# Kernel tuning notes

Measured on AMD Instinct MI355X. Metric: run time of the kernel, lower is better.

The kernel has to match this reference:

```python
import jax, jax.numpy as jnp
import numpy as np

B, C, H, W = 8, 128, 256, 256
KERNELS = [1, 3, 5]


def _dwconv(x, w, k):
    # depthwise conv, groups == channels, padding k//2 (SAME for odd k)
    return jax.lax.conv_general_dilated(
        x, w, window_strides=(1, 1),
        padding=[(k // 2, k // 2), (k // 2, k // 2)],
        dimension_numbers=("NCHW", "OIHW", "NCHW"),
        feature_group_count=x.shape[1])


def setup_inputs() -> dict:
    key = jax.random.key(0)
    ks = jax.random.split(key, 5)
    x = jax.random.normal(ks[0], (B, C, H, W), jnp.float32)
    # depthwise weights: torch layout [out_ch, in_ch/groups, k, k] = [4C, 1, k, k]
    w1 = jax.random.normal(ks[1], (4 * C, 1, 1, 1), jnp.float32) * 0.2
    w3 = jax.random.normal(ks[2], (4 * C, 1, 3, 3), jnp.float32) * 0.1
    w5 = jax.random.normal(ks[3], (4 * C, 1, 5, 5), jnp.float32) * 0.05
    # proj 1x1 conv: [4C, 12C, 1, 1]
    w_proj = jax.random.normal(ks[4], (4 * C, 12 * C, 1, 1), jnp.float32) * 0.02
    return {"x": x, "w1": w1, "w3": w3, "w5": w5, "w_proj": w_proj}


def reference(x, w1, w3, w5, w_proj):
    # DWT: strided split -> channel concat  [B,C,H,W] -> [B,4C,H/2,W/2]
    xd = jnp.concatenate([
        x[:, :, 0::2, 0::2], x[:, :, 0::2, 1::2],
        x[:, :, 1::2, 0::2], x[:, :, 1::2, 1::2]], axis=1)
    # multi-kernel depthwise convs, concat -> [B,12C,H/2,W/2]
    feats = jnp.concatenate([
        _dwconv(xd, w1, 1), _dwconv(xd, w3, 3), _dwconv(xd, w5, 5)], axis=1)
    # 1x1 projection: [B,12C,h,w] -> [B,4C,h,w]
    y = jnp.einsum("bchw,oc->bohw", feats, w_proj[:, :, 0, 0])
    # IDWT: strided zero-scatter back to [B,C,H,W]
    c = y.shape[1] // 4
    ll, lh, hl, hh = jnp.split(y, 4, axis=1)
    out = jnp.zeros((y.shape[0], c, y.shape[2] * 2, y.shape[3] * 2), y.dtype)
    out = (out.at[:, :, 0::2, 0::2].set(ll)
              .at[:, :, 0::2, 1::2].set(lh)
              .at[:, :, 1::2, 0::2].set(hl)
              .at[:, :, 1::2, 1::2].set(hh))
    return out
```

## Files before the change

kernel.cpp:

```cpp
#include <hip/hip_runtime.h>
#include <hip/hip_bf16.h>
#include <stdint.h>

typedef __bf16 bf16_t;
typedef __bf16 bf16x8 __attribute__((ext_vector_type(8)));
typedef float f32x4 __attribute__((ext_vector_type(4)));

constexpr int CC = 128, HH = 256, WW = 256;
constexpr int C4 = 512, K12 = 1536;
constexpr int AWP_ELEMS = 786432;
constexpr int LW2_ELEMS = 512 * 40;

__global__ __launch_bounds__(256)
void prep(const float* __restrict__ wp, const float* __restrict__ w1,
          const float* __restrict__ w3, const float* __restrict__ w5,
          bf16_t* __restrict__ awp, float* __restrict__ lw2g)
{
    int t = blockIdx.x * 256 + threadIdx.x;
    if (t < AWP_ELEMS) {
        int kk = t & 31, o = (t >> 5) & 511, t2 = t >> 14;
        int g = t2 >> 4, cb = t2 & 15;
        awp[t] = (bf16_t)wp[o * K12 + g * C4 + cb * 32 + kk];
        return;
    }
    int u = t - AWP_ELEMS;
    if (u < LW2_ELEMS) {
        int c4 = u / 40, j = u - c4 * 40;
        int r = j >> 3, v = j & 7;
        float val = 0.f;
        if (v < 5)                 val = w5[c4 * 25 + r * 5 + v];
        else if (r >= 1 && r <= 3) val = w3[c4 * 9 + (r - 1) * 3 + (v - 5)];
        else if (r == 0 && v == 5) val = w1[c4];
        lw2g[u] = val;
    }
}

__device__ __forceinline__ void gload4(const float* g, float* l) {
    __builtin_amdgcn_global_load_lds(
        (const __attribute__((address_space(1))) uint32_t*)g,
        (__attribute__((address_space(3))) uint32_t*)l, 4, 0, 0);
}
__device__ __forceinline__ uint16_t b16bits(float v) {
    return __builtin_bit_cast(uint16_t, (bf16_t)v);
}

__device__ __forceinline__ int bt_off(int row, int colbyte) {
    int f = ((row >> 1) ^ (row >> 2)) & 7;
    return row * 256 + (colbyte ^ (f << 4));
}

__global__ __launch_bounds__(1024, 4)
void wtconv_mfma(const float* __restrict__ x,
                 const bf16_t* __restrict__ awp,
                 const float* __restrict__ lw2g,
                 float* __restrict__ out)
{
    __shared__ __align__(16) float lx[32][5][136];
    __shared__ __align__(16) char  BtB[2][128 * 256];
    __shared__ __align__(16) float lw2s[32][40];

    const int tid = threadIdx.x;
    const int lane = tid & 63;
    const int wid = __builtin_amdgcn_readfirstlane(tid >> 6);
    const int nb = blockIdx.x;
    const int m = (nb & 7) * 128 + (nb >> 3);
    const int b = m >> 7, i = m & 127;
    const int wm = wid & 7, wn = wid >> 3;
    const int lrow = lane & 15, lkh = lane >> 4;
    const float* xb = x + (size_t)b * CC * HH * WW;

    for (int e = tid; e < 32 * 5 * 136 / 4; e += 1024)
        ((f32x4*)lx)[e] = (f32x4){0.f, 0.f, 0.f, 0.f};
    __syncthreads();

    f32x4 acc[4][4];
#pragma unroll
    for (int a = 0; a < 4; ++a)
#pragma unroll
        for (int c = 0; c < 4; ++c) acc[a][c] = (f32x4){0.f, 0.f, 0.f, 0.f};

    auto issue_own = [&](int kk) {
        const int q4 = kk >> 2, qy = q4 >> 1, qx = q4 & 1;
        const int bcb = (kk & 3) * 32;
#pragma unroll
        for (int cl = 0; cl < 2; ++cl) {
            const int chan = wid * 2 + cl;
#pragma unroll
            for (int r = 0; r < 5; ++r) {
                const int ri = i + r - 2;
                if ((unsigned)ri < 128u) {
                    const float* s = xb + (((size_t)(bcb + chan)) << 16)
                                   + (2 * ri + qy) * WW + qx;
                    gload4(s + 2 * lane,       &lx[chan][r][2]);
                    gload4(s + 128 + 2 * lane, &lx[chan][r][66]);
                }
            }
        }
        const float* wsrc = lw2g + kk * 1280 + wid * 80;
        float* wdst = &lw2s[wid * 2][0];
        gload4(wsrc + lane, wdst);
        if (lane < 16) gload4(wsrc + 64 + lane, wdst + 64);
    };

    issue_own(0);

    const int chan = tid >> 5;
    const int pxq = tid & 31;
    const int px0 = pxq * 4;

#pragma unroll 1
    for (int k = 0; k <= 16; ++k) {
        __syncthreads();

        if (k < 16) {
            const float* wr = &lw2s[chan][0];
            float f5[4] = {0.f,0.f,0.f,0.f}, f3[4] = {0.f,0.f,0.f,0.f}, f1[4];
            float w1v = 0.f;
#pragma unroll
            for (int r = 0; r < 5; ++r) {
                f32x4 wA = *(const f32x4*)(wr + r * 8);
                f32x4 wB = *(const f32x4*)(wr + r * 8 + 4);
                f32x4 a  = *(const f32x4*)&lx[chan][r][px0];
                f32x4 bv = *(const f32x4*)&lx[chan][r][px0 + 4];
                float c[8] = {a[0],a[1],a[2],a[3],bv[0],bv[1],bv[2],bv[3]};
                if (r == 0) w1v = wB[1];
#pragma unroll
                for (int d = 0; d < 4; ++d)
                    f5[d] += wA[0]*c[d] + wA[1]*c[d+1] + wA[2]*c[d+2]
                           + wA[3]*c[d+3] + wB[0]*c[d+4];
                if (r >= 1 && r <= 3) {
#pragma unroll
                    for (int d = 0; d < 4; ++d)
                        f3[d] += wB[1]*c[d+1] + wB[2]*c[d+2] + wB[3]*c[d+3];
                }
                if (r == 2) {
#pragma unroll
                    for (int d = 0; d < 4; ++d) f1[d] = w1v * c[d + 2];
                }
            }
            char* btb = BtB[k & 1];
            const int cby = chan * 2;
#pragma unroll
            for (int d = 0; d < 4; ++d) {
                const int row = px0 + d;
                const int sw = (((row >> 1) ^ (row >> 2)) & 7) << 4;
                char* base = btb + row * 256;
                *(uint16_t*)(base + ((cby) ^ sw))        = b16bits(f1[d]);
                *(uint16_t*)(base + ((64 + cby) ^ sw))   = b16bits(f3[d]);
                *(uint16_t*)(base + ((128 + cby) ^ sw))  = b16bits(f5[d]);
            }
            if (k < 15) issue_own(k + 1);
        }

        if (k > 0) {
            const int prev = k - 1;
            const char* btb = BtB[prev & 1];
#pragma unroll
            for (int s = 0; s < 3; ++s) {
                bf16x8 bfrag[4];
#pragma unroll
                for (int nf = 0; nf < 4; ++nf) {
                    const int row = wn * 64 + nf * 16 + lrow;
                    const int sw = (((row >> 1) ^ (row >> 2)) & 7) << 4;
                    bfrag[nf] = *(const bf16x8*)(btb + row * 256
                                                 + ((s * 64 + lkh * 16) ^ sw));
                }
                const bf16_t* abase = awp + (size_t)(s * 16 + prev) * (512 * 32);
#pragma unroll
                for (int mf = 0; mf < 4; ++mf) {
                    const int o = wm * 64 + mf * 16 + lrow;
                    bf16x8 af = *(const bf16x8*)(abase + o * 32 + lkh * 8);
#pragma unroll
                    for (int nf = 0; nf < 4; ++nf)
                        acc[mf][nf] = __builtin_amdgcn_mfma_f32_16x16x32_bf16(
                            af, bfrag[nf], acc[mf][nf], 0, 0, 0);
                }
            }
        }
    }

    const int oy = 2 * i + (wm >> 2);
    const int ox = (wm >> 1) & 1;
#pragma unroll
    for (int mf = 0; mf < 4; ++mf)
#pragma unroll
        for (int nf = 0; nf < 4; ++nf)
#pragma unroll
            for (int r = 0; r < 4; ++r) {
                const int bco = (wm & 1) * 64 + mf * 16 + lkh * 4 + r;
                const int px  = wn * 64 + nf * 16 + lrow;
                out[((size_t)(b * CC + bco) * HH + oy) * WW + 2 * px + ox]
                    = acc[mf][nf][r];
            }
}

extern "C" void kernel_launch(void* const* d_in, const int* in_sizes, int n_in,
                              void* d_out, int out_size, void* d_ws, size_t ws_size,
                              hipStream_t stream) {
    const float* x  = (const float*)d_in[0];
    const float* w1 = (const float*)d_in[1];
    const float* w3 = (const float*)d_in[2];
    const float* w5 = (const float*)d_in[3];
    const float* wp = (const float*)d_in[4];
    float* out = (float*)d_out;
    bf16_t* awp = (bf16_t*)d_ws;
    float* lw2g = (float*)((char*)d_ws + (size_t)AWP_ELEMS * 2);

    int prep_total = AWP_ELEMS + LW2_ELEMS;
    hipLaunchKernelGGL(prep, dim3((prep_total + 255) / 256), dim3(256), 0, stream,
                       wp, w1, w3, w5, awp, lw2g);
    hipLaunchKernelGGL(wtconv_mfma, dim3(1024), dim3(1024), 0, stream,
                       x, awp, lw2g, out);
}
```

Before: 514.8 us.

## Warp-specialize block: producer waves do dwconv plus partial MFMA, others MFMA only

Splits the 16 waves into two roles. Waves 0-7 load x tiles, compute the depthwise convolutions into the bf16 B tile, and handle 48 pixel columns of the projection GEMM. Waves 8-15 do only MFMA work on the remaining 80 columns, balancing the producers' extra load. It also changes the LDS swizzle pattern and raises wave priority around the MFMA sections with s_setprio. The aim is to overlap VALU conv work with matrix-core work, at the cost of uneven per-wave register use and a wider per-thread conv footprint.

Result: slower. 580.9 us (+12.9%).

```diff
diff --git a/kernel.cpp b/kernel.cpp
--- a/kernel.cpp
+++ b/kernel.cpp
@@ -43,10 +43,8 @@
 __device__ __forceinline__ uint16_t b16bits(float v) {
     return __builtin_bit_cast(uint16_t, (bf16_t)v);
 }
-
-__device__ __forceinline__ int bt_off(int row, int colbyte) {
-    int f = ((row >> 1) ^ (row >> 2)) & 7;
-    return row * 256 + (colbyte ^ (f << 4));
+__device__ __forceinline__ int btsw(int row) {
+    return (((row >> 1) ^ (row >> 3)) & 7) << 4;
 }
 
 __global__ __launch_bounds__(1024, 4)
@@ -65,7 +63,6 @@
     const int nb = blockIdx.x;
     const int m = (nb & 7) * 128 + (nb >> 3);
     const int b = m >> 7, i = m & 127;
-    const int wm = wid & 7, wn = wid >> 3;
     const int lrow = lane & 15, lkh = lane >> 4;
     const float* xb = x + (size_t)b * CC * HH * WW;
 
@@ -73,125 +70,180 @@
         ((f32x4*)lx)[e] = (f32x4){0.f, 0.f, 0.f, 0.f};
     __syncthreads();
 
-    f32x4 acc[4][4];
-#pragma unroll
-    for (int a = 0; a < 4; ++a)
-#pragma unroll
-        for (int c = 0; c < 4; ++c) acc[a][c] = (f32x4){0.f, 0.f, 0.f, 0.f};
-
-    auto issue_own = [&](int kk) {
-        const int q4 = kk >> 2, qy = q4 >> 1, qx = q4 & 1;
-        const int bcb = (kk & 3) * 32;
-#pragma unroll
-        for (int cl = 0; cl < 2; ++cl) {
-            const int chan = wid * 2 + cl;
-#pragma unroll
-            for (int r = 0; r < 5; ++r) {
-                const int ri = i + r - 2;
-                if ((unsigned)ri < 128u) {
-                    const float* s = xb + (((size_t)(bcb + chan)) << 16)
-                                   + (2 * ri + qy) * WW + qx;
-                    gload4(s + 2 * lane,       &lx[chan][r][2]);
-                    gload4(s + 128 + 2 * lane, &lx[chan][r][66]);
+    if (wid < 8) {
+        f32x4 acc[4][3];
+#pragma unroll
+        for (int a = 0; a < 4; ++a)
+#pragma unroll
+            for (int c = 0; c < 3; ++c) acc[a][c] = (f32x4){0.f, 0.f, 0.f, 0.f};
+
+        auto issue_own = [&](int kk) {
+            const int q4 = kk >> 2, qy = q4 >> 1, qx = q4 & 1;
+            const int bcb = (kk & 3) * 32;
+#pragma unroll
+            for (int cl = 0; cl < 4; ++cl) {
+                const int ch = wid * 4 + cl;
+#pragma unroll
+                for (int r = 0; r < 5; ++r) {
+                    const int ri = i + r - 2;
+                    if ((unsigned)ri < 128u) {
+                        const float* s = xb + (((size_t)(bcb + ch)) << 16)
+                                       + (2 * ri + qy) * WW + qx;
+                        gload4(s + 2 * lane,       &lx[ch][r][2]);
+                        gload4(s + 128 + 2 * lane, &lx[ch][r][66]);
+                    }
+                }
+            }
+            const float* wsrc = lw2g + kk * 1280 + wid * 160;
+            float* wdst = &lw2s[wid * 4][0];
+            gload4(wsrc + lane, wdst);
+            gload4(wsrc + 64 + lane, wdst + 64);
+            if (lane < 32) gload4(wsrc + 128 + lane, wdst + 128);
+        };
+        issue_own(0);
+
+        const int chan = wid * 4 + (lane >> 4);
+        const int oct = lane & 15;
+        const int px0 = oct * 8;
+
+#pragma unroll 1
+        for (int k = 0; k <= 16; ++k) {
+            __syncthreads();
+
+            if (k < 16) {
+                const float* wrow = &lw2s[chan][0];
+                float f5[8] = {0,0,0,0,0,0,0,0}, f3[8] = {0,0,0,0,0,0,0,0}, f1[8];
+                float w1v = 0.f;
+#pragma unroll
+                for (int r = 0; r < 5; ++r) {
+                    f32x4 wA = *(const f32x4*)(wrow + r * 8);
+                    f32x4 wB = *(const f32x4*)(wrow + r * 8 + 4);
+                    f32x4 v0 = *(const f32x4*)&lx[chan][r][px0];
+                    f32x4 v1 = *(const f32x4*)&lx[chan][r][px0 + 4];
+                    f32x4 v2 = *(const f32x4*)&lx[chan][r][px0 + 8];
+                    float cc[12] = {v0[0],v0[1],v0[2],v0[3], v1[0],v1[1],v1[2],v1[3],
+                                    v2[0],v2[1],v2[2],v2[3]};
+                    if (r == 0) w1v = wB[1];
+#pragma unroll
+                    for (int d = 0; d < 8; ++d)
+                        f5[d] += wA[0]*cc[d] + wA[1]*cc[d+1] + wA[2]*cc[d+2]
+                               + wA[3]*cc[d+3] + wB[0]*cc[d+4];
+                    if (r >= 1 && r <= 3) {
+#pragma unroll
+                        for (int d = 0; d < 8; ++d)
+                            f3[d] += wB[1]*cc[d+1] + wB[2]*cc[d+2] + wB[3]*cc[d+3];
+                    }
+                    if (r == 2) {
+#pragma unroll
+                        for (int d = 0; d < 8; ++d) f1[d] = w1v * cc[d + 2];
+                    }
+                }
+                char* btb = BtB[k & 1];
+                const int cby = chan * 2;
+#pragma unroll
+                for (int d = 0; d < 8; ++d) {
+                    const int row = px0 + d;
+                    char* base = btb + row * 256;
+                    const int sw = btsw(row);
+                    *(uint16_t*)(base + ((cby) ^ sw))       = b16bits(f1[d]);
+                    *(uint16_t*)(base + ((64 + cby) ^ sw))  = b16bits(f3[d]);
+                    *(uint16_t*)(base + ((128 + cby) ^ sw)) = b16bits(f5[d]);
+                }
+                if (k < 15) issue_own(k + 1);
+            }
+
+            if (k > 0) {
+                const int prev = k - 1;
+                const char* btb = BtB[prev & 1];
+#pragma unroll
+                for (int s = 0; s < 3; ++s) {
+                    bf16x8 bfrag[3];
+#pragma unroll
+                    for (int nf = 0; nf < 3; ++nf) {
+                        const int row = nf * 16 + lrow;
+                        bfrag[nf] = *(const bf16x8*)(btb + row * 256
+                                       + ((s * 64 + lkh * 16) ^ btsw(row)));
+                    }
+                    const bf16_t* abase = awp + (size_t)(s * 16 + prev) * (512 * 32);
+                    __builtin_amdgcn_s_setprio(1);
+#pragma unroll
+                    for (int mf = 0; mf < 4; ++mf) {
+                        const int o = wid * 64 + mf * 16 + lrow;
+                        bf16x8 af = *(const bf16x8*)(abase + o * 32 + lkh * 8);
+#pragma unroll
+                        for (int nf = 0; nf < 3; ++nf)
+                            acc[mf][nf] = __builtin_amdgcn_mfma_f32_16x16x32_bf16(
+                                af, bfrag[nf], acc[mf][nf], 0, 0, 0);
+                    }
+                    __builtin_amdgcn_s_setprio(0);
                 }
             }
         }
-        const float* wsrc = lw2g + kk * 1280 + wid * 80;
-        float* wdst = &lw2s[wid * 2][0];
-        gload4(wsrc + lane, wdst);
-        if (lane < 16) gload4(wsrc + 64 + lane, wdst + 64);
-    };
-
-    issue_own(0);
-
-    const int chan = tid >> 5;
-    const int pxq = tid & 31;
-    const int px0 = pxq * 4;
+        const int q = wid >> 1;
+        const int oy = 2 * i + (q >> 1), ox = q & 1;
+#pragma unroll
+        for (int mf = 0; mf < 4; ++mf)
+#pragma unroll
+            for (int nf = 0; nf < 3; ++nf)
+#pragma unroll
+                for (int r = 0; r < 4; ++r) {
+                    const int bco = (wid & 1) * 64 + mf * 16 + lkh * 4 + r;
+                    const int px  = nf * 16 + lrow;
+                    out[((size_t)(b * CC + bco) * HH + oy) * WW + 2 * px + ox]
+                        = acc[mf][nf][r];
+                }
+    } else {
+        f32x4 acc[4][5];
+#pragma unroll
+        for (int a = 0; a < 4; ++a)
+#pragma unroll
+            for (int c = 0; c < 5; ++c) acc[a][c] = (f32x4){0.f, 0.f, 0.f, 0.f};
+        const int wmB = wid - 8;
 
 #pragma unroll 1
-    for (int k = 0; k <= 16; ++k) {
-        __syncthreads();
-
-        if (k < 16) {
-            const float* wr = &lw2s[chan][0];
-            float f5[4] = {0.f,0.f,0.f,0.f}, f3[4] = {0.f,0.f,0.f,0.f}, f1[4];
-            float w1v = 0.f;
-#pragma unroll
-            for (int r = 0; r < 5; ++r) {
-                f32x4 wA = *(const f32x4*)(wr + r * 8);
-                f32x4 wB = *(const f32x4*)(wr + r * 8 + 4);
-                f32x4 a  = *(const f32x4*)&lx[chan][r][px0];
-                f32x4 bv = *(const f32x4*)&lx[chan][r][px0 + 4];
-                float c[8] = {a[0],a[1],a[2],a[3],bv[0],bv[1],bv[2],bv[3]};
-                if (r == 0) w1v = wB[1];
-#pragma unroll
-                for (int d = 0; d < 4; ++d)
-                    f5[d] += wA[0]*c[d] + wA[1]*c[d+1] + wA[2]*c[d+2]
-                           + wA[3]*c[d+3] + wB[0]*c[d+4];
-                if (r >= 1 && r <= 3) {
-#pragma unroll
-                    for (int d = 0; d < 4; ++d)
-                        f3[d] += wB[1]*c[d+1] + wB[2]*c[d+2] + wB[3]*c[d+3];
-                }
-                if (r == 2) {
-#pragma unroll
-                    for (int d = 0; d < 4; ++d) f1[d] = w1v * c[d + 2];
-                }
-            }
-            char* btb = BtB[k & 1];
-            const int cby = chan * 2;
-#pragma unroll
-            for (int d = 0; d < 4; ++d) {
-                const int row = px0 + d;
-                const int sw = (((row >> 1) ^ (row >> 2)) & 7) << 4;
-                char* base = btb + row * 256;
-                *(uint16_t*)(base + ((cby) ^ sw))        = b16bits(f1[d]);
-                *(uint16_t*)(base + ((64 + cby) ^ sw))   = b16bits(f3[d]);
-                *(uint16_t*)(base + ((128 + cby) ^ sw))  = b16bits(f5[d]);
-            }
-            if (k < 15) issue_own(k + 1);
+        for (int k = 0; k <= 16; ++k) {
+            __syncthreads();
+            if (k > 0) {
+                const int prev = k - 1;
+                const char* btb = BtB[prev & 1];
+#pragma unroll
+                for (int s = 0; s < 3; ++s) {
+                    bf16x8 bfrag[5];
+#pragma unroll
+                    for (int nf = 0; nf < 5; ++nf) {
+                        const int row = 48 + nf * 16 + lrow;
+                        bfrag[nf] = *(const bf16x8*)(btb + row * 256
+                                       + ((s * 64 + lkh * 16) ^ btsw(row)));
+                    }
+                    const bf16_t* abase = awp + (size_t)(s * 16 + prev) * (512 * 32);
+                    __builtin_amdgcn_s_setprio(1);
+#pragma unroll
+                    for (int mf = 0; mf < 4; ++mf) {
+                        const int o = wmB * 64 + mf * 16 + lrow;
+                        bf16x8 af = *(const bf16x8*)(abase + o * 32 + lkh * 8);
+#pragma unroll
+                        for (int nf = 0; nf < 5; ++nf)
+                            acc[mf][nf] = __builtin_amdgcn_mfma_f32_16x16x32_bf16(
+                                af, bfrag[nf], acc[mf][nf], 0, 0, 0);
+                    }
+                    __builtin_amdgcn_s_setprio(0);
+                }
+            }
         }
-
-        if (k > 0) {
-            const int prev = k - 1;
-            const char* btb = BtB[prev & 1];
-#pragma unroll
-            for (int s = 0; s < 3; ++s) {
-                bf16x8 bfrag[4];
-#pragma unroll
-                for (int nf = 0; nf < 4; ++nf) {
-                    const int row = wn * 64 + nf * 16 + lrow;
-                    const int sw = (((row >> 1) ^ (row >> 2)) & 7) << 4;
-                    bfrag[nf] = *(const bf16x8*)(btb + row * 256
-                                                 + ((s * 64 + lkh * 16) ^ sw));
-                }
-                const bf16_t* abase = awp + (size_t)(s * 16 + prev) * (512 * 32);
-#pragma unroll
-                for (int mf = 0; mf < 4; ++mf) {
-                    const int o = wm * 64 + mf * 16 + lrow;
-                    bf16x8 af = *(const bf16x8*)(abase + o * 32 + lkh * 8);
-#pragma unroll
-                    for (int nf = 0; nf < 4; ++nf)
-                        acc[mf][nf] = __builtin_amdgcn_mfma_f32_16x16x32_bf16(
-                            af, bfrag[nf], acc[mf][nf], 0, 0, 0);
-                }
-            }
-        }
+        const int q = wmB >> 1;
+        const int oy = 2 * i + (q >> 1), ox = q & 1;
+#pragma unroll
+        for (int mf = 0; mf < 4; ++mf)
+#pragma unroll
+            for (int nf = 0; nf < 5; ++nf)
+#pragma unroll
+                for (int r = 0; r < 4; ++r) {
+                    const int bco = (wmB & 1) * 64 + mf * 16 + lkh * 4 + r;
+                    const int px  = 48 + nf * 16 + lrow;
+                    out[((size_t)(b * CC + bco) * HH + oy) * WW + 2 * px + ox]
+                        = acc[mf][nf][r];
+                }
     }
-
-    const int oy = 2 * i + (wm >> 2);
-    const int ox = (wm >> 1) & 1;
-#pragma unroll
-    for (int mf = 0; mf < 4; ++mf)
-#pragma unroll
-        for (int nf = 0; nf < 4; ++nf)
-#pragma unroll
-            for (int r = 0; r < 4; ++r) {
-                const int bco = (wm & 1) * 64 + mf * 16 + lkh * 4 + r;
-                const int px  = wn * 64 + nf * 16 + lrow;
-                out[((size_t)(b * CC + bco) * HH + oy) * WW + 2 * px + ox]
-                    = acc[mf][nf][r];
-            }
 }
 
 extern "C" void kernel_launch(void* const* d_in, const int* in_sizes, int n_in,
```

## Specialize half the waves for depthwise conv and raise MFMA issue priority

Applied to the files above, without the earlier changes.

The depthwise-conv producer stage moves from all 16 waves to only the first 8. Each of those waves now loads 4 channels and computes 8 pixels per thread, while the other 8 waves only run MFMAs. The LDS swizzle for the B tile changes to match the new write pattern, and s_setprio brackets the MFMA section so matrix ops get issue priority. The aim is to reuse each loaded input window across more outputs and to overlap conv with MFMA. The risks are more register pressure, idle waves during the conv stage, and an imbalance between the two groups.

New measurement: 821.1 us. 1.6x slower.

```diff
diff --git a/kernel.cpp b/kernel.cpp
--- a/kernel.cpp
+++ b/kernel.cpp
@@ -43,10 +43,8 @@
 __device__ __forceinline__ uint16_t b16bits(float v) {
     return __builtin_bit_cast(uint16_t, (bf16_t)v);
 }
-
-__device__ __forceinline__ int bt_off(int row, int colbyte) {
-    int f = ((row >> 1) ^ (row >> 2)) & 7;
-    return row * 256 + (colbyte ^ (f << 4));
+__device__ __forceinline__ int btsw(int row) {
+    return (((row >> 1) ^ (row >> 3)) & 7) << 4;
 }
 
 __global__ __launch_bounds__(1024, 4)
@@ -83,71 +81,73 @@
         const int q4 = kk >> 2, qy = q4 >> 1, qx = q4 & 1;
         const int bcb = (kk & 3) * 32;
 #pragma unroll
-        for (int cl = 0; cl < 2; ++cl) {
-            const int chan = wid * 2 + cl;
+        for (int cl = 0; cl < 4; ++cl) {
+            const int ch = wid * 4 + cl;
 #pragma unroll
             for (int r = 0; r < 5; ++r) {
                 const int ri = i + r - 2;
                 if ((unsigned)ri < 128u) {
-                    const float* s = xb + (((size_t)(bcb + chan)) << 16)
+                    const float* s = xb + (((size_t)(bcb + ch)) << 16)
                                    + (2 * ri + qy) * WW + qx;
-                    gload4(s + 2 * lane,       &lx[chan][r][2]);
-                    gload4(s + 128 + 2 * lane, &lx[chan][r][66]);
+                    gload4(s + 2 * lane,       &lx[ch][r][2]);
+                    gload4(s + 128 + 2 * lane, &lx[ch][r][66]);
                 }
             }
         }
-        const float* wsrc = lw2g + kk * 1280 + wid * 80;
-        float* wdst = &lw2s[wid * 2][0];
+        const float* wsrc = lw2g + kk * 1280 + wid * 160;
+        float* wdst = &lw2s[wid * 4][0];
         gload4(wsrc + lane, wdst);
-        if (lane < 16) gload4(wsrc + 64 + lane, wdst + 64);
+        gload4(wsrc + 64 + lane, wdst + 64);
+        if (lane < 32) gload4(wsrc + 128 + lane, wdst + 128);
     };
 
-    issue_own(0);
-
-    const int chan = tid >> 5;
-    const int pxq = tid & 31;
-    const int px0 = pxq * 4;
+    if (wid < 8) issue_own(0);
+
+    const int cchan = wid * 4 + (lane >> 4);
+    const int px0 = (lane & 15) * 8;
 
 #pragma unroll 1
     for (int k = 0; k <= 16; ++k) {
         __syncthreads();
 
-        if (k < 16) {
-            const float* wr = &lw2s[chan][0];
-            float f5[4] = {0.f,0.f,0.f,0.f}, f3[4] = {0.f,0.f,0.f,0.f}, f1[4];
+        if (wid < 8 && k < 16) {
+            const float* wr = &lw2s[cchan][0];
+            float f5[8] = {0,0,0,0,0,0,0,0}, f3[8] = {0,0,0,0,0,0,0,0}, f1[8];
             float w1v = 0.f;
 #pragma unroll
             for (int r = 0; r < 5; ++r) {
                 f32x4 wA = *(const f32x4*)(wr + r * 8);
                 f32x4 wB = *(const f32x4*)(wr + r * 8 + 4);
-                f32x4 a  = *(const f32x4*)&lx[chan][r][px0];
-                f32x4 bv = *(const f32x4*)&lx[chan][r][px0 + 4];
-                float c[8] = {a[0],a[1],a[2],a[3],bv[0],bv[1],bv[2],bv[3]};
+                f32x4 v0 = *(const f32x4*)&lx[cchan][r][px0];
+                f32x4 v1 = *(const f32x4*)&lx[cchan][r][px0 + 4];
+                f32x4 v2 = *(const f32x4*)&lx[cchan][r][px0 + 8];
+                float cc[12] = {v0[0],v0[1],v0[2],v0[3], v1[0],v1[1],v1[2],v1[3],
+                                v2[0],v2[1],v2[2],v2[3]};
                 if (r == 0) w1v = wB[1];
 #pragma unroll
-                for (int d = 0; d < 4; ++d)
-                    f5[d] += wA[0]*c[d] + wA[1]*c[d+1] + wA[2]*c[d+2]
-                           + wA[3]*c[d+3] + wB[0]*c[d+4];
+                for (int d = 0; d < 8; ++d)
+                    f5[d] += wA[0]*cc[d] + wA[1]*cc[d+1] + wA[2]*cc[d+2]
+                           + wA[3]*cc[d+3] + wB[0]*cc[d+4];
                 if (r >= 1 && r <= 3) {
 #pragma unroll
-                    for (int d = 0; d < 4; ++d)
-                        f3[d] += wB[1]*c[d+1] + wB[2]*c[d+2] + wB[3]*c[d+3];
+                    for (int d = 0; d < 8; ++d)
+                        f3[d] += wB[1]*cc[d+1] + wB[2]*cc[d+2] + wB[3]*cc[d+3];
                 }
                 if (r == 2) {
 #pragma unroll
-                    for (int d = 0; d < 4; ++d) f1[d] = w1v * c[d + 2];
+                    for (int d = 0; d < 8; ++d) f1[d] = w1v * cc[d + 2];
                 }
             }
             char* btb = BtB[k & 1];
-            const int cby = chan * 2;
-#pragma unroll
-            for (int d = 0; d < 4; ++d) {
+            const int cby = cchan * 2;
+#pragma unroll
+            for (int d = 0; d < 8; ++d) {
                 const int row = px0 + d;
-                const int sw = (((row >> 1) ^ (row >> 2)) & 7) << 4;
+                const int sw = btsw(row);
                 char* base = btb + row * 256;
-                *(uint16_t*)(base + ((cby) ^ sw))        = b16bits(f1[d]);
-                *(uint16_t*)(base + ((64 + cby) ^ sw))   = b16bits(f3[d]);
-                *(uint16_t*)(base + ((128 + cby) ^ sw))  = b16bits(f5[d]);
+                *(uint16_t*)(base + ((cby) ^ sw))       = b16bits(f1[d]);
+                *(uint16_t*)(base + ((64 + cby) ^ sw))  = b16bits(f3[d]);
+                *(uint16_t*)(base + ((128 + cby) ^ sw)) = b16bits(f5[d]);
             }
             if (k < 15) issue_own(k + 1);
         }
@@ -161,11 +161,11 @@
 #pragma unroll
                 for (int nf = 0; nf < 4; ++nf) {
                     const int row = wn * 64 + nf * 16 + lrow;
-                    const int sw = (((row >> 1) ^ (row >> 2)) & 7) << 4;
                     bfrag[nf] = *(const bf16x8*)(btb + row * 256
-                                                 + ((s * 64 + lkh * 16) ^ sw));
+                                                 + ((s * 64 + lkh * 16) ^ btsw(row)));
                 }
                 const bf16_t* abase = awp + (size_t)(s * 16 + prev) * (512 * 32);
+                __builtin_amdgcn_s_setprio(1);
 #pragma unroll
                 for (int mf = 0; mf < 4; ++mf) {
                     const int o = wm * 64 + mf * 16 + lrow;
@@ -175,6 +175,7 @@
                         acc[mf][nf] = __builtin_amdgcn_mfma_f32_16x16x32_bf16(
                             af, bfrag[nf], acc[mf][nf], 0, 0, 0);
                 }
+                __builtin_amdgcn_s_setprio(0);
             }
         }
     }
```

## Split each output row across two 512-thread blocks with halo loads

Applied to the files above, without the earlier changes.

Each block now covers half of a downsampled row (64 pixels) with 512 threads instead of the full row with 1024 threads, and the grid doubles to 2048 blocks. Shared buffers shrink to match, each wave loads 4 channels, and two-element halo columns are fetched from the neighbouring half. Block-to-batch mapping changes so consecutive blocks span batches. MFMA sections are wrapped in s_setprio. The aim is more resident blocks and better latency hiding; the cost is that the projection weight (A) fragments are re-read by twice as many blocks and halo loads are duplicated.

Result: no change. 520.1 us (+1.0%).

```diff
diff --git a/kernel.cpp b/kernel.cpp
--- a/kernel.cpp
+++ b/kernel.cpp
@@ -43,33 +43,32 @@
 __device__ __forceinline__ uint16_t b16bits(float v) {
     return __builtin_bit_cast(uint16_t, (bf16_t)v);
 }
-
-__device__ __forceinline__ int bt_off(int row, int colbyte) {
-    int f = ((row >> 1) ^ (row >> 2)) & 7;
-    return row * 256 + (colbyte ^ (f << 4));
-}
-
-__global__ __launch_bounds__(1024, 4)
+__device__ __forceinline__ int btsw(int row) {
+    return (((row >> 1) ^ (row >> 2)) & 7) << 4;
+}
+
+__global__ __launch_bounds__(512, 4)
 void wtconv_mfma(const float* __restrict__ x,
                  const bf16_t* __restrict__ awp,
                  const float* __restrict__ lw2g,
                  float* __restrict__ out)
 {
-    __shared__ __align__(16) float lx[32][5][136];
-    __shared__ __align__(16) char  BtB[2][128 * 256];
+    __shared__ __align__(16) float lx[32][5][68];
+    __shared__ __align__(16) char  BtB[2][64 * 256];
     __shared__ __align__(16) float lw2s[32][40];
 
     const int tid = threadIdx.x;
     const int lane = tid & 63;
     const int wid = __builtin_amdgcn_readfirstlane(tid >> 6);
     const int nb = blockIdx.x;
-    const int m = (nb & 7) * 128 + (nb >> 3);
-    const int b = m >> 7, i = m & 127;
-    const int wm = wid & 7, wn = wid >> 3;
+    const int b = nb & 7;
+    const int t = nb >> 3;
+    const int i = t >> 1;
+    const int half = t & 1;
     const int lrow = lane & 15, lkh = lane >> 4;
     const float* xb = x + (size_t)b * CC * HH * WW;
 
-    for (int e = tid; e < 32 * 5 * 136 / 4; e += 1024)
+    for (int e = tid; e < 32 * 5 * 68 / 4; e += 512)
         ((f32x4*)lx)[e] = (f32x4){0.f, 0.f, 0.f, 0.f};
     __syncthreads();
 
@@ -83,29 +82,35 @@
         const int q4 = kk >> 2, qy = q4 >> 1, qx = q4 & 1;
         const int bcb = (kk & 3) * 32;
 #pragma unroll
-        for (int cl = 0; cl < 2; ++cl) {
-            const int chan = wid * 2 + cl;
+        for (int cl = 0; cl < 4; ++cl) {
+            const int ch = wid * 4 + cl;
 #pragma unroll
             for (int r = 0; r < 5; ++r) {
                 const int ri = i + r - 2;
                 if ((unsigned)ri < 128u) {
-                    const float* s = xb + (((size_t)(bcb + chan)) << 16)
-                                   + (2 * ri + qy) * WW + qx;
-                    gload4(s + 2 * lane,       &lx[chan][r][2]);
-                    gload4(s + 128 + 2 * lane, &lx[chan][r][66]);
+                    const float* srow = xb + (((size_t)(bcb + ch)) << 16)
+                                      + (2 * ri + qy) * WW + qx;
+                    gload4(srow + 2 * (half * 64 + lane), &lx[ch][r][2]);
+                    if (lane < 2) {
+                        if (half == 0)
+                            gload4(srow + 2 * (64 + lane), &lx[ch][r][66]);
+                        else
+                            gload4(srow + 2 * (62 + lane), &lx[ch][r][0]);
+                    }
                 }
             }
         }
-        const float* wsrc = lw2g + kk * 1280 + wid * 80;
-        float* wdst = &lw2s[wid * 2][0];
+        const float* wsrc = lw2g + kk * 1280 + wid * 160;
+        float* wdst = &lw2s[wid * 4][0];
         gload4(wsrc + lane, wdst);
-        if (lane < 16) gload4(wsrc + 64 + lane, wdst + 64);
+        gload4(wsrc + 64 + lane, wdst + 64);
+        if (lane < 32) gload4(wsrc + 128 + lane, wdst + 128);
     };
 
     issue_own(0);
 
-    const int chan = tid >> 5;
-    const int pxq = tid & 31;
+    const int chan = tid >> 4;
+    const int pxq = tid & 15;
     const int px0 = pxq * 4;
 
 #pragma unroll 1
@@ -143,7 +148,7 @@
 #pragma unroll
             for (int d = 0; d < 4; ++d) {
                 const int row = px0 + d;
-                const int sw = (((row >> 1) ^ (row >> 2)) & 7) << 4;
+                const int sw = btsw(row);
                 char* base = btb + row * 256;
                 *(uint16_t*)(base + ((cby) ^ sw))        = b16bits(f1[d]);
                 *(uint16_t*)(base + ((64 + cby) ^ sw))   = b16bits(f3[d]);
@@ -160,35 +165,36 @@
                 bf16x8 bfrag[4];
 #pragma unroll
                 for (int nf = 0; nf < 4; ++nf) {
-                    const int row = wn * 64 + nf * 16 + lrow;
-                    const int sw = (((row >> 1) ^ (row >> 2)) & 7) << 4;
+                    const int row = nf * 16 + lrow;
                     bfrag[nf] = *(const bf16x8*)(btb + row * 256
-                                                 + ((s * 64 + lkh * 16) ^ sw));
+                                                 + ((s * 64 + lkh * 16) ^ btsw(row)));
                 }
                 const bf16_t* abase = awp + (size_t)(s * 16 + prev) * (512 * 32);
+                __builtin_amdgcn_s_setprio(1);
 #pragma unroll
                 for (int mf = 0; mf < 4; ++mf) {
-                    const int o = wm * 64 + mf * 16 + lrow;
+                    const int o = wid * 64 + mf * 16 + lrow;
                     bf16x8 af = *(const bf16x8*)(abase + o * 32 + lkh * 8);
 #pragma unroll
                     for (int nf = 0; nf < 4; ++nf)
                         acc[mf][nf] = __builtin_amdgcn_mfma_f32_16x16x32_bf16(
                             af, bfrag[nf], acc[mf][nf], 0, 0, 0);
                 }
+                __builtin_amdgcn_s_setprio(0);
             }
         }
     }
 
-    const int oy = 2 * i + (wm >> 2);
-    const int ox = (wm >> 1) & 1;
+    const int q = wid >> 1;
+    const int oy = 2 * i + (q >> 1), ox = q & 1;
 #pragma unroll
     for (int mf = 0; mf < 4; ++mf)
 #pragma unroll
         for (int nf = 0; nf < 4; ++nf)
 #pragma unroll
             for (int r = 0; r < 4; ++r) {
-                const int bco = (wm & 1) * 64 + mf * 16 + lkh * 4 + r;
-                const int px  = wn * 64 + nf * 16 + lrow;
+                const int bco = (wid & 1) * 64 + mf * 16 + lkh * 4 + r;
+                const int px  = half * 64 + nf * 16 + lrow;
                 out[((size_t)(b * CC + bco) * HH + oy) * WW + 2 * px + ox]
                     = acc[mf][nf][r];
             }
@@ -209,6 +215,6 @@
     int prep_total = AWP_ELEMS + LW2_ELEMS;
     hipLaunchKernelGGL(prep, dim3((prep_total + 255) / 256), dim3(256), 0, stream,
                        wp, w1, w3, w5, awp, lw2g);
-    hipLaunchKernelGGL(wtconv_mfma, dim3(1024), dim3(1024), 0, stream,
+    hipLaunchKernelGGL(wtconv_mfma, dim3(2048), dim3(512), 0, stream,
                        x, awp, lw2g, out);
 }
```
